# Kernel tuning notes

Hardware: AMD Instinct MI355X
Metric: run time of the kernel (lower is better)

Reference implementation:

```python
import jax, jax.numpy as jnp
import numpy as np

H = 512      # hidden_size
L = 3        # num_layers
V = 4        # vocab / input_size
E = 64       # embedding_dim
B = 64       # batch
T = 512      # sequence length


def _rnn_layer(xs, h0, w_ih, w_hh, b_ih, b_hh):
    # xs: [T, B, D_in], h0: [B, H] -> (ys [T,B,H], hT [B,H])
    def step(h, x):
        h_new = jnp.tanh(x @ w_ih.T + b_ih + h @ w_hh.T + b_hh)
        return h_new, h_new
    hT, ys = jax.lax.scan(step, h0, xs)
    return ys, hT


def setup_inputs() -> dict:
    key = jax.random.key(0)
    ks = jax.random.split(key, 12)
    s = 1.0 / np.sqrt(H)  # torch RNN default init scale
    inp = {
        "x": jax.random.normal(ks[0], (B, T, V), dtype=jnp.float32),
        "emb": jax.random.normal(ks[1], (V, E), dtype=jnp.float32),
        # encoder RNN: layer 0 has input dim E, layers 1..2 have input dim H
        "enc_w_ih0": jax.random.uniform(ks[2], (H, E), jnp.float32, -s, s),
        "enc_w_ih_rest": jax.random.uniform(ks[3], (L - 1, H, H), jnp.float32, -s, s),
        "enc_w_hh": jax.random.uniform(ks[4], (L, H, H), jnp.float32, -s, s),
        "enc_b_ih": jax.random.uniform(ks[5], (L, H), jnp.float32, -s, s),
        "enc_b_hh": jax.random.uniform(ks[6], (L, H), jnp.float32, -s, s),
        # decoder RNN: all layers have input dim H
        "dec_w_ih": jax.random.uniform(ks[7], (L, H, H), jnp.float32, -s, s),
        "dec_w_hh": jax.random.uniform(ks[8], (L, H, H), jnp.float32, -s, s),
        "dec_b_ih": jax.random.uniform(ks[9], (L, H), jnp.float32, -s, s),
        "dec_b_hh": jax.random.uniform(ks[10], (L, H), jnp.float32, -s, s),
        "proj_w": jax.random.uniform(ks[11], (V, H), jnp.float32, -s, s),
    }
    return inp


def reference(x, emb, enc_w_ih0, enc_w_ih_rest, enc_w_hh, enc_b_ih, enc_b_hh,
              dec_w_ih, dec_w_hh, dec_b_ih, dec_b_hh, proj_w):
    # ---- Encoder ----
    # x_reduced_info slice is empty (FIRST_NONFUNCTIONAL_REDUCED_TOKEN_INDEX == len(VOCAB_REDUCED)),
    # so encoder RNN input is just the embedding of argmax(x).
    idx = jnp.argmax(x, axis=2)            # [B, T] int
    e = emb[idx]                           # [B, T, E]
    xs = jnp.transpose(e, (1, 0, 2))       # [T, B, E] (time-major for scan)

    h0 = jnp.zeros((B, H), dtype=x.dtype)
    enc_finals = []
    ys, hT = _rnn_layer(xs, h0, enc_w_ih0, enc_w_hh[0], enc_b_ih[0], enc_b_hh[0])
    enc_finals.append(hT)
    for l in range(1, L):
        ys, hT = _rnn_layer(ys, h0, enc_w_ih_rest[l - 1], enc_w_hh[l], enc_b_ih[l], enc_b_hh[l])
        enc_finals.append(hT)
    enc_h = jnp.stack(enc_finals, axis=0)  # [L, B, H]

    dec_h0 = jnp.flip(enc_h, axis=0)       # reverse_input_h=True
    x0 = jnp.zeros((B, H), dtype=x.dtype)

    def dec_step(carry, _):
        xin, hs = carry                    # xin [B,H], hs [L,B,H]
        new_hs = []
        cur = xin
        for l in range(L):
            h = jnp.tanh(cur @ dec_w_ih[l].T + dec_b_ih[l]
                         + hs[l] @ dec_w_hh[l].T + dec_b_hh[l])
            new_hs.append(h)
            cur = h
        out = jax.nn.log_softmax(cur @ proj_w.T, axis=-1)  # [B, V]
        return (cur, jnp.stack(new_hs, axis=0)), out

    _, outs = jax.lax.scan(dec_step, (x0, dec_h0), None, length=T)  # [T, B, V]
    return jnp.transpose(outs, (1, 0, 2))  # [B, T, V]
```

## Files before the change

kernel.cpp:

```cpp
#include <hip/hip_runtime.h>
#include <cmath>

#define HH 512
#define NV 4
#define ED 64
#define NB 64
#define NT 512

#define NWG  256
#define NTHR 512
#define WPG  32
#define RPG  8
#define CPW  16

#define HPAR (NB * HH)

#define IN0_OFF 0
#define IN1_OFF (8 * 1024)
#define LDS_FLOATS (IN1_OFF + 8 * 1024)
#define LDS_BYTES_ALLOC 98304

#define WS_INT_FLOATS 9216
#define FLAG(g, cb) (((g) * 32 + (cb)) * 32)

static __device__ __forceinline__ float gld(const float* p) {
  return __hip_atomic_load(p, __ATOMIC_RELAXED, __HIP_MEMORY_SCOPE_AGENT);
}
static __device__ __forceinline__ void gst(float* p, float v) {
  __hip_atomic_store(p, v, __ATOMIC_RELAXED, __HIP_MEMORY_SCOPE_AGENT);
}

static __device__ __forceinline__ void gbar_arrive(int* flags, int g, int cb,
                                                   int ph) {
  asm volatile("s_waitcnt vmcnt(0)" ::: "memory");
  __syncthreads();
  if (threadIdx.x == 0)
    __hip_atomic_store(flags + FLAG(g, cb), ph, __ATOMIC_RELAXED,
                       __HIP_MEMORY_SCOPE_AGENT);
}
static __device__ __forceinline__ void gbar_wait(int* flags, int g, int ph) {
  if (threadIdx.x < 64) {
    const int* f = flags + FLAG(g, threadIdx.x & 31);
    while (__hip_atomic_load(f, __ATOMIC_RELAXED,
                             __HIP_MEMORY_SCOPE_AGENT) < ph)
      __builtin_amdgcn_s_sleep(1);
  }
  __syncthreads();
  asm volatile("" ::: "memory");
}
static __device__ __forceinline__ void gbar(int* flags, int g, int cb, int ph) {
  gbar_arrive(flags, g, cb, ph);
  gbar_wait(flags, g, ph);
}

static __device__ __forceinline__ void gbar_all(int* ctr) {
  asm volatile("s_waitcnt vmcnt(0)" ::: "memory");
  __syncthreads();
  if (threadIdx.x == 0) {
    __hip_atomic_fetch_add(ctr, 1, __ATOMIC_RELAXED, __HIP_MEMORY_SCOPE_AGENT);
    while (__hip_atomic_load(ctr, __ATOMIC_RELAXED,
                             __HIP_MEMORY_SCOPE_AGENT) < NWG)
      __builtin_amdgcn_s_sleep(1);
  }
  __syncthreads();
  asm volatile("" ::: "memory");
}

template <bool COH>
static __device__ __forceinline__ void half_issue(const float* src, int row0,
                                                  float4 (&v)[2]) {
#pragma unroll
  for (int j = 0; j < 2; ++j) {
    const int qq = threadIdx.x + NTHR * j;
    const int row = qq >> 7, kq = qq & 127;
    const float* p = src + (size_t)(row0 + row) * HH + (kq << 2);
    if (COH) asm volatile("global_load_dwordx4 %0, %1, off sc0" : "=v"(v[j]) : "v"(p));
    else     asm volatile("global_load_dwordx4 %0, %1, off sc0 sc1" : "=v"(v[j]) : "v"(p));
  }
}
static __device__ __forceinline__ void half_commit(float* lds, int off,
                                                   int kofs, const float4 (&v)[2]) {
#pragma unroll
  for (int j = 0; j < 2; ++j) {
    const int qq = threadIdx.x + NTHR * j;
    const int row = qq >> 7, kq = qq & 127;
    *(float4*)(lds + off + row * 1024 + kofs + (kq << 2)) = v[j];
  }
}
static __device__ __forceinline__ void stage_half(float* lds, int off,
                                                  const float* src, int row0,
                                                  int kofs, int coh) {
  float4 v[2];
  if (coh) half_issue<true>(src, row0, v);
  else     half_issue<false>(src, row0, v);
  asm volatile("s_waitcnt vmcnt(0)" ::: "memory");
  __builtin_amdgcn_sched_barrier(0);
  half_commit(lds, off, kofs, v);
}

#define PF_DRAIN() \
  do { asm volatile("s_waitcnt vmcnt(0)" ::: "memory"); \
       __builtin_amdgcn_sched_barrier(0); } while (0)

static __device__ __forceinline__ void unpk(float (&w)[16], int q, float4 v) {
  w[4*q+0] = v.x; w[4*q+1] = v.y; w[4*q+2] = v.z; w[4*q+3] = v.w;
}
static __device__ __forceinline__ void load_wq(float (&w)[16], const float* ih,
                                               const float* hh, int col, int ks) {
  unpk(w, 0, *(const float4*)(ih + (size_t)col * HH + ks * 4));
  unpk(w, 1, *(const float4*)(ih + (size_t)col * HH + 256 + ks * 4));
  unpk(w, 2, *(const float4*)(hh + (size_t)col * HH + ks * 4));
  unpk(w, 3, *(const float4*)(hh + (size_t)col * HH + 256 + ks * 4));
}
static __device__ __forceinline__ void load_wq0(float (&w)[16], const float* e,
                                                const float* hh, int col, int ks) {
  const float4 z = make_float4(0.f, 0.f, 0.f, 0.f);
  unpk(w, 0, (ks < 16) ? *(const float4*)(e + (size_t)col * ED + ks * 4)
                       : *(const float4*)(hh + (size_t)col * HH + (ks * 4 - 64)));
  unpk(w, 1, *(const float4*)(hh + (size_t)col * HH + 192 + ks * 4));
  unpk(w, 2, (ks < 16) ? *(const float4*)(hh + (size_t)col * HH + 448 + ks * 4) : z);
  unpk(w, 3, z);
}

static __device__ __forceinline__ void tile_acc2(
    float (&a)[16], const float* lds, int tile_off, int q0,
    const float (&wA)[16], const float (&wB)[16]) {
  const int lane = threadIdx.x & 63;
  const float* base = lds + tile_off + lane * 4;
#pragma unroll
  for (int r = 0; r < 8; ++r) {
    const float* rb = base + r * 1024;
#pragma unroll
    for (int qq = 0; qq < 2; ++qq) {
      const int q = q0 + qq;
      const float4 iv = *(const float4*)(rb + q * 256);
      a[2*r+0] = fmaf(wA[4*q+0], iv.x, a[2*r+0]);
      a[2*r+0] = fmaf(wA[4*q+1], iv.y, a[2*r+0]);
      a[2*r+0] = fmaf(wA[4*q+2], iv.z, a[2*r+0]);
      a[2*r+0] = fmaf(wA[4*q+3], iv.w, a[2*r+0]);
      a[2*r+1] = fmaf(wB[4*q+0], iv.x, a[2*r+1]);
      a[2*r+1] = fmaf(wB[4*q+1], iv.y, a[2*r+1]);
      a[2*r+1] = fmaf(wB[4*q+2], iv.z, a[2*r+1]);
      a[2*r+1] = fmaf(wB[4*q+3], iv.w, a[2*r+1]);
    }
  }
}
static __device__ __forceinline__ void zero16(float (&a)[16]) {
#pragma unroll
  for (int v = 0; v < 16; ++v) a[v] = 0.f;
}

static __device__ __forceinline__ void tile_finish(
    float (&a)[16], float bA, float bB,
    float* dst, float* dst2, int row0, int colA, int coh) {
  const int lane = threadIdx.x & 63;
#pragma unroll
  for (int i = 0; i < 8; ++i) {
    const float send = (lane & 32) ? a[i] : a[i + 8];
    const float recv = __shfl_xor(send, 32);
    const float keep = (lane & 32) ? a[i + 8] : a[i];
    a[i] = keep + recv;
  }
#pragma unroll
  for (int i = 0; i < 4; ++i) {
    const float send = (lane & 16) ? a[i] : a[i + 4];
    const float recv = __shfl_xor(send, 16);
    const float keep = (lane & 16) ? a[i + 4] : a[i];
    a[i] = keep + recv;
  }
#pragma unroll
  for (int i = 0; i < 2; ++i) {
    const float send = (lane & 8) ? a[i] : a[i + 2];
    const float recv = __shfl_xor(send, 8);
    const float keep = (lane & 8) ? a[i + 2] : a[i];
    a[i] = keep + recv;
  }
  {
    const float send = (lane & 4) ? a[0] : a[1];
    const float recv = __shfl_xor(send, 4);
    const float keep = (lane & 4) ? a[1] : a[0];
    a[0] = keep + recv;
  }
  a[0] += __shfl_xor(a[0], 1);
  a[0] += __shfl_xor(a[0], 2);
  if ((lane & 3) == 0) {
    const int r  = ((lane >> 5) & 1) * 4 + ((lane >> 4) & 1) * 2 + ((lane >> 3) & 1);
    const int cc = (lane >> 2) & 1;
    const float h = tanhf(a[0] + (cc ? bB : bA));
    const size_t idx = (size_t)(row0 + r) * HH + colA + cc;
    if (coh) { dst[idx] = h; if (dst2) dst2[idx] = h; }
    else     { gst(dst + idx, h); if (dst2) gst(dst2 + idx, h); }
  }
}

static __device__ __forceinline__ void layer_tile(
    float* lds, int tile_off,
    const float (&wA)[16], const float (&wB)[16], float bA, float bB,
    float* dst, float* dst2, int row0, int colA, int coh) {
  __syncthreads();
  float a[16];
  zero16(a);
  tile_acc2(a, lds, tile_off, 0, wA, wB);
  tile_acc2(a, lds, tile_off, 2, wA, wB);
  __syncthreads();
  tile_finish(a, bA, bB, dst, dst2, row0, colA, coh);
}

static __device__ __forceinline__ void proj_row(const float* lds, int tile_off,
                                                int r_local, const float* projw,
                                                float* out, int row, int tt) {
  const int lane = threadIdx.x;
  const int v = lane & 3, kq = lane >> 2;
  float acc = 0.f;
#pragma unroll
  for (int i8 = 0; i8 < 8; ++i8) {
    const int k = (kq << 5) + (i8 << 2);
    const float4 iv = *(const float4*)(lds + tile_off + r_local * 1024 + k);
    const float4 wv = *(const float4*)(projw + (size_t)v * HH + k);
    acc = fmaf(iv.x, wv.x, acc);
    acc = fmaf(iv.y, wv.y, acc);
    acc = fmaf(iv.z, wv.z, acc);
    acc = fmaf(iv.w, wv.w, acc);
  }
  acc += __shfl_xor(acc, 4);
  acc += __shfl_xor(acc, 8);
  acc += __shfl_xor(acc, 16);
  acc += __shfl_xor(acc, 32);
  float m = fmaxf(acc, __shfl_xor(acc, 1));
  m = fmaxf(m, __shfl_xor(m, 2));
  const float e = expf(acc - m);
  float sum = e + __shfl_xor(e, 1);
  sum += __shfl_xor(sum, 2);
  const float res = acc - m - logf(sum);
  if (lane < 4) out[((size_t)row * NT + tt) * NV + lane] = res;
}

#define STG(off, src, kofs) stage_half(lds, off, src, row0, kofs, coh)
#define PF_ISSUE(src) \
  do { if (coh) half_issue<true>(src, row0, pf); \
       else     half_issue<false>(src, row0, pf); } while (0)

__global__ void __launch_bounds__(NTHR, 2) rnn_ae(
    const float* __restrict__ x, const float* __restrict__ emb,
    const float* __restrict__ ew_ih0, const float* __restrict__ ew_ihr,
    const float* __restrict__ ew_hh, const float* __restrict__ eb_ih,
    const float* __restrict__ eb_hh,
    const float* __restrict__ dw_ih, const float* __restrict__ dw_hh,
    const float* __restrict__ db_ih, const float* __restrict__ db_hh,
    const float* __restrict__ projw,
    float* __restrict__ out, float* __restrict__ ws) {
  extern __shared__ float lds[];

  const int tid = threadIdx.x;
  const int bid = blockIdx.x;
  const int c   = tid >> 6;
  const int ks  = tid & 63;

  int* flags  = (int*)ws;
  int* gctr   = (int*)ws + 8192;
  int* xcdtab = (int*)ws + 8704;
  float* h0  = ws + WS_INT_FLOATS;
  float* h1  = h0 + 2 * HPAR;
  float* h2  = h1 + 2 * HPAR;
  float* e0  = h2 + 2 * HPAR;
  float* e1  = e0 + 2 * HPAR;
  float* e2  = e1 + 2 * HPAR;
  float* xfb = e2 + 2 * HPAR;
  int ph = 0;

  unsigned xcc;
  asm volatile("s_getreg_b32 %0, hwreg(HW_REG_XCC_ID)" : "=s"(xcc));
  if (tid == 0)
    __hip_atomic_store(xcdtab + bid, (int)xcc, __ATOMIC_RELAXED,
                       __HIP_MEMORY_SCOPE_AGENT);

  for (int i = tid; i < LDS_FLOATS; i += NTHR) lds[i] = 0.f;
  {
    const int zg = bid & 7, zcb = bid >> 3;
    for (int i = zcb * NTHR + tid; i < RPG * HH; i += WPG * NTHR) {
      const int r = i >> 9, cc = i & 511;
      const size_t o = HPAR + (size_t)(zg * RPG + r) * HH + cc;
      gst(h0 + o, 0.f); gst(h1 + o, 0.f); gst(h2 + o, 0.f);
    }
  }

  gbar_all(gctr);

  int g, cb, coh;
  {
    int* ldsX = (int*)(lds + IN1_OFF);
    if (tid < NWG)
      ldsX[tid] = __hip_atomic_load(xcdtab + tid, __ATOMIC_RELAXED,
                                    __HIP_MEMORY_SCOPE_AGENT);
    __syncthreads();
    const int myx = ldsX[bid] & 7;
    unsigned long long cnt = 0;
    int rank = 0;
    for (int b = 0; b < NWG; ++b) {
      const int xb = ldsX[b] & 7;
      cnt += 1ull << (xb * 8);
      if (b < bid && xb == myx) ++rank;
    }
    if (cnt == 0x2020202020202020ull) {
      g = myx; cb = rank; coh = 1;
    } else {
      g = bid & 7; cb = bid >> 3;
      coh = 1;
      const int x0 = ldsX[g] & 7;
      for (int j = 1; j < WPG; ++j)
        coh &= ((ldsX[g + 8 * j] & 7) == x0);
    }
    __syncthreads();
  }
  const int row0 = g * RPG;
  const int col0 = cb * CPW;
  const int colA = col0 + 2 * c;
  const int colB = colA + 1;

  float wA0[16], wB0[16], wA1[16], wB1[16], wA2[16], wB2[16];
  float bA0, bB0, bA1, bB1, bA2, bB2;
  load_wq0(wA0, ew_ih0, ew_hh, colA, ks);
  load_wq0(wB0, ew_ih0, ew_hh, colB, ks);
  load_wq(wA1, ew_ihr,                ew_hh + (size_t)HH * HH,     colA, ks);
  load_wq(wB1, ew_ihr,                ew_hh + (size_t)HH * HH,     colB, ks);
  load_wq(wA2, ew_ihr + (size_t)HH * HH, ew_hh + (size_t)2 * HH * HH, colA, ks);
  load_wq(wB2, ew_ihr + (size_t)HH * HH, ew_hh + (size_t)2 * HH * HH, colB, ks);
  bA0 = eb_ih[0*HH + colA] + eb_hh[0*HH + colA];
  bB0 = eb_ih[0*HH + colB] + eb_hh[0*HH + colB];
  bA1 = eb_ih[1*HH + colA] + eb_hh[1*HH + colA];
  bB1 = eb_ih[1*HH + colB] + eb_hh[1*HH + colB];
  bA2 = eb_ih[2*HH + colA] + eb_hh[2*HH + colA];
  bB2 = eb_ih[2*HH + colB] + eb_hh[2*HH + colB];

  for (int s = 0; s < NT + 2; ++s) {
    const int t = s, t1 = s - 1, t2 = s - 2;
    float4 v0[2], v1a[2], v1b[2], v2a[2], v2b[2];
    if (s < NT) {
      if (coh) half_issue<true>(h0 + ((t&1)^1) * HPAR, row0, v0);
      else     half_issue<false>(h0 + ((t&1)^1) * HPAR, row0, v0);
    }
    if (s >= 1 && s < NT + 1) {
      if (coh) { half_issue<true>(h0 + (t1&1) * HPAR, row0, v1a);
                 half_issue<true>(h1 + ((t1&1)^1) * HPAR, row0, v1b); }
      else     { half_issue<false>(h0 + (t1&1) * HPAR, row0, v1a);
                 half_issue<false>(h1 + ((t1&1)^1) * HPAR, row0, v1b); }
    }
    if (s >= 2) {
      if (coh) { half_issue<true>(h1 + (t2&1) * HPAR, row0, v2a);
                 half_issue<true>(h2 + ((t2&1)^1) * HPAR, row0, v2b); }
      else     { half_issue<false>(h1 + (t2&1) * HPAR, row0, v2a);
                 half_issue<false>(h2 + ((t2&1)^1) * HPAR, row0, v2b); }
    }
    asm volatile("s_waitcnt vmcnt(0)" ::: "memory");
    __builtin_amdgcn_sched_barrier(0);

    if (s < NT) {
      half_commit(lds, IN0_OFF, 64, v0);
      if (tid < 128) {
        const int r = tid >> 4, i8 = tid & 15;
        const float* xr = x + ((size_t)(row0 + r) * NT + t) * NV;
        const float a0 = xr[0], a1 = xr[1], a2 = xr[2], a3 = xr[3];
        int idx = 0; float m = a0;
        if (a1 > m) { m = a1; idx = 1; }
        if (a2 > m) { m = a2; idx = 2; }
        if (a3 > m) { m = a3; idx = 3; }
        const int k = i8 << 2;
        *(float4*)(lds + IN0_OFF + r * 1024 + k) =
            *(const float4*)(emb + idx * ED + k);
      }
    }
    if (s >= 1 && s < NT + 1) {
      half_commit(lds, IN1_OFF, 0,   v1a);
      half_commit(lds, IN1_OFF, 512, v1b);
    }
    if (s < NT)
      layer_tile(lds, IN0_OFF, wA0, wB0, bA0, bB0,
                 h0 + (t&1) * HPAR, nullptr, row0, colA, coh);
    if (s >= 1 && s < NT + 1)
      layer_tile(lds, IN1_OFF, wA1, wB1, bA1, bB1,
                 h1 + (t1&1) * HPAR, nullptr, row0, colA, coh);
    if (s >= 2) {
      half_commit(lds, IN1_OFF, 0,   v2a);
      half_commit(lds, IN1_OFF, 512, v2b);
      layer_tile(lds, IN1_OFF, wA2, wB2, bA2, bB2,
                 h2 + (t2&1) * HPAR, nullptr, row0, colA, coh);
    }
    gbar(flags, g, cb, ++ph);
  }

  for (int i = cb * NTHR + tid; i < RPG * HH; i += WPG * NTHR) {
    const int r = i >> 9, cc = i & 511;
    const size_t o = HPAR + (size_t)(row0 + r) * HH + cc;
    const float a = gld(h2 + o);
    const float b = gld(h1 + o);
    const float cv = gld(h0 + o);
    if (coh) { e0[o] = a; e1[o] = b; e2[o] = cv; xfb[o] = 0.f; }
    else     { gst(e0 + o, a); gst(e1 + o, b); gst(e2 + o, cv); gst(xfb + o, 0.f); }
  }
  load_wq(wA0, dw_ih,                     dw_hh,                     colA, ks);
  load_wq(wB0, dw_ih,                     dw_hh,                     colB, ks);
  load_wq(wA1, dw_ih + (size_t)HH * HH,   dw_hh + (size_t)HH * HH,   colA, ks);
  load_wq(wB1, dw_ih + (size_t)HH * HH,   dw_hh + (size_t)HH * HH,   colB, ks);
  load_wq(wA2, dw_ih + (size_t)2*HH*HH,   dw_hh + (size_t)2*HH*HH,   colA, ks);
  load_wq(wB2, dw_ih + (size_t)2*HH*HH,   dw_hh + (size_t)2*HH*HH,   colB, ks);
  bA0 = db_ih[0*HH + colA] + db_hh[0*HH + colA];
  bB0 = db_ih[0*HH + colB] + db_hh[0*HH + colB];
  bA1 = db_ih[1*HH + colA] + db_hh[1*HH + colA];
  bB1 = db_ih[1*HH + colB] + db_hh[1*HH + colB];
  bA2 = db_ih[2*HH + colA] + db_hh[2*HH + colA];
  bB2 = db_ih[2*HH + colB] + db_hh[2*HH + colB];
  gbar(flags, g, cb, ++ph);

  float4 pf[2];
  {
    const int p = 0, q = 1;
    STG(IN1_OFF, e0 + q * HPAR, 512);
    STG(IN1_OFF, xfb + q * HPAR, 0);
    __syncthreads();
    layer_tile(lds, IN1_OFF, wA0, wB0, bA0, bB0, e0 + p * HPAR, nullptr,
               row0, colA, coh);
    PF_ISSUE(e1 + q * HPAR);
    gbar(flags, g, cb, ++ph);

    half_commit(lds, IN1_OFF, 512, pf);
    STG(IN1_OFF, e0 + p * HPAR, 0);
    __syncthreads();
    layer_tile(lds, IN1_OFF, wA1, wB1, bA1, bB1, e1 + p * HPAR, nullptr,
               row0, colA, coh);
    PF_ISSUE(e2 + q * HPAR);
    gbar(flags, g, cb, ++ph);

    half_commit(lds, IN1_OFF, 512, pf);
    STG(IN1_OFF, e1 + p * HPAR, 0);
    __syncthreads();
    layer_tile(lds, IN1_OFF, wA2, wB2, bA2, bB2, e2 + p * HPAR,
               xfb + p * HPAR, row0, colA, coh);
    PF_ISSUE(e0 + p * HPAR);
    gbar(flags, g, cb, ++ph);
  }

  for (int t = 1; t < NT; ++t) {
    const int p = t & 1, q = p ^ 1;

    PF_DRAIN();
    half_commit(lds, IN1_OFF, 512, pf);
    __syncthreads();
    float a0[16]; zero16(a0);
    tile_acc2(a0, lds, IN1_OFF, 2, wA0, wB0);
    gbar_wait(flags, g, ph);
    STG(IN1_OFF, xfb + q * HPAR, 0);
    __syncthreads();
    if (cb < 8 && tid < 64)
      proj_row(lds, IN1_OFF, cb, projw, out, row0 + cb, t - 1);
    tile_acc2(a0, lds, IN1_OFF, 0, wA0, wB0);
    tile_finish(a0, bA0, bB0, e0 + p * HPAR, nullptr, row0, colA, coh);
    gbar_arrive(flags, g, cb, ++ph);
    PF_ISSUE(e1 + q * HPAR);

    PF_DRAIN();
    half_commit(lds, IN1_OFF, 512, pf);
    __syncthreads();
    float a1[16]; zero16(a1);
    tile_acc2(a1, lds, IN1_OFF, 2, wA1, wB1);
    gbar_wait(flags, g, ph);
    STG(IN1_OFF, e0 + p * HPAR, 0);
    __syncthreads();
    tile_acc2(a1, lds, IN1_OFF, 0, wA1, wB1);
    tile_finish(a1, bA1, bB1, e1 + p * HPAR, nullptr, row0, colA, coh);
    gbar_arrive(flags, g, cb, ++ph);
    PF_ISSUE(e2 + q * HPAR);

    PF_DRAIN();
    half_commit(lds, IN1_OFF, 512, pf);
    __syncthreads();
    float a2[16]; zero16(a2);
    tile_acc2(a2, lds, IN1_OFF, 2, wA2, wB2);
    gbar_wait(flags, g, ph);
    STG(IN1_OFF, e1 + p * HPAR, 0);
    __syncthreads();
    tile_acc2(a2, lds, IN1_OFF, 0, wA2, wB2);
    tile_finish(a2, bA2, bB2, e2 + p * HPAR, xfb + p * HPAR, row0, colA, coh);
    gbar_arrive(flags, g, cb, ++ph);
    PF_ISSUE(e0 + p * HPAR);
  }

  gbar_wait(flags, g, ph);
  STG(IN1_OFF, xfb + ((NT - 1) & 1) * HPAR, 0);
  __syncthreads();
  if (cb < 8 && tid < 64)
    proj_row(lds, IN1_OFF, cb, projw, out, row0 + cb, NT - 1);
}

extern "C" void kernel_launch(void* const* d_in, const int* in_sizes, int n_in,
                              void* d_out, int out_size, void* d_ws, size_t ws_size,
                              hipStream_t stream) {
  const float* x      = (const float*)d_in[0];
  const float* emb    = (const float*)d_in[1];
  const float* ew_ih0 = (const float*)d_in[2];
  const float* ew_ihr = (const float*)d_in[3];
  const float* ew_hh  = (const float*)d_in[4];
  const float* eb_ih  = (const float*)d_in[5];
  const float* eb_hh  = (const float*)d_in[6];
  const float* dw_ih  = (const float*)d_in[7];
  const float* dw_hh  = (const float*)d_in[8];
  const float* db_ih  = (const float*)d_in[9];
  const float* db_hh  = (const float*)d_in[10];
  const float* projw  = (const float*)d_in[11];
  float* out = (float*)d_out;
  float* ws  = (float*)d_ws;

  (void)hipMemsetAsync(d_ws, 0, WS_INT_FLOATS * 4, stream);

  (void)hipFuncSetAttribute((const void*)rnn_ae,
                            hipFuncAttributeMaxDynamicSharedMemorySize,
                            LDS_BYTES_ALLOC);

  rnn_ae<<<dim3(NWG), dim3(NTHR), LDS_BYTES_ALLOC, stream>>>(
      x, emb, ew_ih0, ew_ihr, ew_hh, eb_ih, eb_hh,
      dw_ih, dw_hh, db_ih, db_hh, projw, out, ws);
}
```

Before: 7.021 ms.

## Split encoder grid barrier and overlap recurrent-half matvec with barrier wait

The encoder wavefront loop now splits the grid barrier into arrive and wait. It prefetches the recurrent hidden-state halves for layers 1 and 2 right after arriving, then computes those halves' partial products before waiting on the barrier. A third LDS input buffer (IN2) is added so layers 1 and 2 no longer share staging space, and the ldsX scratch is cleared after rank assignment. The aim is to hide global-barrier latency and load latency behind useful FMA work, at the cost of more LDS use, more register pressure from the extra accumulators, and more intricate ordering assumptions.

```diff
diff --git a/kernel.cpp b/kernel.cpp
--- a/kernel.cpp
+++ b/kernel.cpp
@@ -17,7 +17,8 @@
 
 #define IN0_OFF 0
 #define IN1_OFF (8 * 1024)
-#define LDS_FLOATS (IN1_OFF + 8 * 1024)
+#define IN2_OFF (16 * 1024)
+#define LDS_FLOATS (IN2_OFF + 8 * 1024)
 #define LDS_BYTES_ALLOC 98304
 
 #define WS_INT_FLOATS 9216
@@ -239,6 +240,12 @@
 #define PF_ISSUE(src) \
   do { if (coh) half_issue<true>(src, row0, pf); \
        else     half_issue<false>(src, row0, pf); } while (0)
+#define PF1_ISSUE(src) \
+  do { if (coh) half_issue<true>(src, row0, pf1); \
+       else     half_issue<false>(src, row0, pf1); } while (0)
+#define PF2_ISSUE(src) \
+  do { if (coh) half_issue<true>(src, row0, pf2); \
+       else     half_issue<false>(src, row0, pf2); } while (0)
 
 __global__ void __launch_bounds__(NTHR, 2) rnn_ae(
     const float* __restrict__ x, const float* __restrict__ emb,
@@ -310,6 +317,8 @@
       for (int j = 1; j < WPG; ++j)
         coh &= ((ldsX[g + 8 * j] & 7) == x0);
     }
+    __syncthreads();
+    if (tid < NWG) ldsX[tid] = 0;
     __syncthreads();
   }
   const int row0 = g * RPG;
@@ -332,33 +341,43 @@
   bA2 = eb_ih[2*HH + colA] + eb_hh[2*HH + colA];
   bB2 = eb_ih[2*HH + colB] + eb_hh[2*HH + colB];
 
-  for (int s = 0; s < NT + 2; ++s) {
-    const int t = s, t1 = s - 1, t2 = s - 2;
-    float4 v0[2], v1a[2], v1b[2], v2a[2], v2b[2];
-    if (s < NT) {
-      if (coh) half_issue<true>(h0 + ((t&1)^1) * HPAR, row0, v0);
-      else     half_issue<false>(h0 + ((t&1)^1) * HPAR, row0, v0);
-    }
-    if (s >= 1 && s < NT + 1) {
-      if (coh) { half_issue<true>(h0 + (t1&1) * HPAR, row0, v1a);
-                 half_issue<true>(h1 + ((t1&1)^1) * HPAR, row0, v1b); }
-      else     { half_issue<false>(h0 + (t1&1) * HPAR, row0, v1a);
-                 half_issue<false>(h1 + ((t1&1)^1) * HPAR, row0, v1b); }
-    }
-    if (s >= 2) {
-      if (coh) { half_issue<true>(h1 + (t2&1) * HPAR, row0, v2a);
-                 half_issue<true>(h2 + ((t2&1)^1) * HPAR, row0, v2b); }
-      else     { half_issue<false>(h1 + (t2&1) * HPAR, row0, v2a);
-                 half_issue<false>(h2 + ((t2&1)^1) * HPAR, row0, v2b); }
-    }
-    asm volatile("s_waitcnt vmcnt(0)" ::: "memory");
-    __builtin_amdgcn_sched_barrier(0);
-
-    if (s < NT) {
+  float4 pf1[2], pf2[2];
+  for (int s = 0; s <= NT + 1; ++s) {
+    const bool l0a = s < NT;
+    const bool l1a = (s >= 1) && (s < NT + 1);
+    const bool l2a = s >= 2;
+
+    if (l1a || l2a) {
+      PF_DRAIN();
+      if (l1a) half_commit(lds, IN1_OFF, 512, pf1);
+      if (l2a) half_commit(lds, IN2_OFF, 512, pf2);
+      __syncthreads();
+    }
+    float A0[16], A1[16], A2[16];
+    if (l1a) { zero16(A1); tile_acc2(A1, lds, IN1_OFF, 2, wA1, wB1); }
+
+    gbar_wait(flags, g, ph);
+
+    float4 v0[2], v1a[2], v2a[2];
+    if (l0a) {
+      if (coh) half_issue<true>(h0 + ((s&1)^1) * HPAR, row0, v0);
+      else     half_issue<false>(h0 + ((s&1)^1) * HPAR, row0, v0);
+    }
+    if (l1a) {
+      if (coh) half_issue<true>(h0 + ((s-1)&1) * HPAR, row0, v1a);
+      else     half_issue<false>(h0 + ((s-1)&1) * HPAR, row0, v1a);
+    }
+    if (l2a) {
+      if (coh) half_issue<true>(h1 + ((s-2)&1) * HPAR, row0, v2a);
+      else     half_issue<false>(h1 + ((s-2)&1) * HPAR, row0, v2a);
+    }
+    if (l2a) { zero16(A2); tile_acc2(A2, lds, IN2_OFF, 2, wA2, wB2); }
+    PF_DRAIN();
+    if (l0a) {
       half_commit(lds, IN0_OFF, 64, v0);
       if (tid < 128) {
         const int r = tid >> 4, i8 = tid & 15;
-        const float* xr = x + ((size_t)(row0 + r) * NT + t) * NV;
+        const float* xr = x + ((size_t)(row0 + r) * NT + s) * NV;
         const float a0 = xr[0], a1 = xr[1], a2 = xr[2], a3 = xr[3];
         int idx = 0; float m = a0;
         if (a1 > m) { m = a1; idx = 1; }
@@ -369,24 +388,30 @@
             *(const float4*)(emb + idx * ED + k);
       }
     }
-    if (s >= 1 && s < NT + 1) {
-      half_commit(lds, IN1_OFF, 0,   v1a);
-      half_commit(lds, IN1_OFF, 512, v1b);
-    }
-    if (s < NT)
-      layer_tile(lds, IN0_OFF, wA0, wB0, bA0, bB0,
-                 h0 + (t&1) * HPAR, nullptr, row0, colA, coh);
-    if (s >= 1 && s < NT + 1)
-      layer_tile(lds, IN1_OFF, wA1, wB1, bA1, bB1,
-                 h1 + (t1&1) * HPAR, nullptr, row0, colA, coh);
-    if (s >= 2) {
-      half_commit(lds, IN1_OFF, 0,   v2a);
-      half_commit(lds, IN1_OFF, 512, v2b);
-      layer_tile(lds, IN1_OFF, wA2, wB2, bA2, bB2,
-                 h2 + (t2&1) * HPAR, nullptr, row0, colA, coh);
-    }
-    gbar(flags, g, cb, ++ph);
-  }
+    if (l1a) half_commit(lds, IN1_OFF, 0, v1a);
+    if (l2a) half_commit(lds, IN2_OFF, 0, v2a);
+    __syncthreads();
+
+    if (l0a) {
+      zero16(A0);
+      tile_acc2(A0, lds, IN0_OFF, 0, wA0, wB0);
+      tile_acc2(A0, lds, IN0_OFF, 2, wA0, wB0);
+      tile_finish(A0, bA0, bB0, h0 + (s&1) * HPAR, nullptr, row0, colA, coh);
+    }
+    if (l1a) {
+      tile_acc2(A1, lds, IN1_OFF, 0, wA1, wB1);
+      tile_finish(A1, bA1, bB1, h1 + ((s-1)&1) * HPAR, nullptr, row0, colA, coh);
+    }
+    if (l2a) {
+      tile_acc2(A2, lds, IN2_OFF, 0, wA2, wB2);
+      tile_finish(A2, bA2, bB2, h2 + ((s-2)&1) * HPAR, nullptr, row0, colA, coh);
+    }
+
+    gbar_arrive(flags, g, cb, ++ph);
+    if (s < NT)             PF1_ISSUE(h1 + ((s&1)^1) * HPAR);
+    if (s >= 1 && s <= NT)  PF2_ISSUE(h2 + (((s-1)&1)^1) * HPAR);
+  }
+  gbar_wait(flags, g, ph);
 
   for (int i = cb * NTHR + tid; i < RPG * HH; i += WPG * NTHR) {
     const int r = i >> 9, cc = i & 511;
```

Result: slower. 7.162 ms (+2.0%).
